# Kernel optimization log

Hardware: AMD Instinct MI355X
Metric: run time of the kernel (lower is better)

Reference implementation:

```python
import jax, jax.numpy as jnp
import numpy as np
import math

B, I, H = 8192, 1024, 1024

def _uniform(key, shape, lo, hi):
    return jax.random.uniform(key, shape, dtype=jnp.float32, minval=lo, maxval=hi)

def setup_inputs() -> dict:
    key = jax.random.key(0)
    ks = jax.random.split(key, 14)
    bound = math.sqrt(1.0 / H)
    lo, hi = -bound, bound
    x = jax.random.normal(ks[0], (B, I), dtype=jnp.float32)
    hid = jax.random.normal(ks[1], (B, H), dtype=jnp.float32)
    # stacked params for gates [r, z, n]
    wx = jnp.stack([_uniform(ks[2 + i], (I, H), lo, hi) for i in range(3)])   # [3, I, H]
    wh = jnp.stack([_uniform(ks[5 + i], (H, H), lo, hi) for i in range(3)])   # [3, H, H]
    bx = jnp.stack([_uniform(ks[8 + i], (H,), lo, hi) for i in range(3)])     # [3, H]
    bh = jnp.stack([_uniform(ks[11 + i], (H,), lo, hi) for i in range(3)])    # [3, H]
    return {"x": x, "hid": hid, "wx": wx, "wh": wh, "bx": bx, "bh": bh}

def reference(x, hid, wx, wh, bx, bh):
    # Fused gate projections: one big matmul per source instead of 3 small ones.
    gx = jnp.einsum('bi,gih->bgh', x, wx) + bx[None]        # [B, 3, H]
    gh = jnp.einsum('bh,ghk->bgk', hid, wh) + bh[None]      # [B, 3, H]
    r = jax.nn.sigmoid(gx[:, 0] + gh[:, 0])
    z = jax.nn.sigmoid(gx[:, 1] + gh[:, 1])
    n = jnp.tanh(gx[:, 2] + r * gh[:, 2])
    next_hid = (1.0 - z) * n + z * hid
    return next_hid
```

## Files before the change

kernel.cpp:

```cpp
#include <hip/hip_runtime.h>
#include <hip/hip_bf16.h>

typedef __hip_bfloat16 bf16;
typedef unsigned short u16;
typedef __attribute__((ext_vector_type(8))) short bf16x8;
typedef __attribute__((ext_vector_type(4))) float f32x4;
typedef __attribute__((ext_vector_type(8))) unsigned short u16x8;

#define KD 1024
#define HD 1024
#define BSZ 8192
#define BM 128
#define BN 64
#define BK 32

#define WS_XB 12582912
#define WS_HB 29360128
#define WS_NEED 46137344ULL

#define NTRB 1536

__device__ __forceinline__ u16 f2b(float f) {
    return __builtin_bit_cast(u16, __float2bfloat16(f));
}

__device__ __forceinline__ void gload16(const void* g, u16* smem, int lds_byte_off) {
    __builtin_amdgcn_global_load_lds(
        (const __attribute__((address_space(1))) void*)g,
        (__attribute__((address_space(3))) void*)((char*)smem + lds_byte_off),
        16, 0, 0);
}

__global__ __launch_bounds__(256) void prep(
    const float* __restrict__ wx, const float* __restrict__ wh, u16* __restrict__ wt,
    const float* __restrict__ x, const float* __restrict__ h,
    u16* __restrict__ xb, u16* __restrict__ hb)
{
    __shared__ float tile[64 * 69];
    const int b = blockIdx.x;
    const int t = threadIdx.x;

    if (b < NTRB) {
        const int g  = b >> 8;
        const int rm = b & 255;
        const int r0 = (rm >> 4) * 64;
        const int c0 = (rm & 15) * 64;
        const float* src = (g < 3) ? (wx + (size_t)g * KD * HD)
                                   : (wh + (size_t)(g - 3) * KD * HD);
        u16* dst = wt + (size_t)g * KD * HD;

        #pragma unroll
        for (int ps = 0; ps < 4; ps++) {
            int idx = ps * 256 + t;
            int row = idx >> 4;
            int c4  = (idx & 15) * 4;
            float4 v = *(const float4*)(src + (size_t)(r0 + row) * HD + c0 + c4);
            *(float4*)&tile[row * 69 + c4] = v;
        }
        __syncthreads();
        const int n = t >> 2;
        #pragma unroll
        for (int p = 0; p < 2; p++) {
            int k0 = (t & 3) * 8 + p * 32;
            u16x8 v;
            #pragma unroll
            for (int e = 0; e < 8; e++)
                v[e] = f2b(tile[(k0 + e) * 69 + n]);
            *(u16x8*)(dst + (size_t)(c0 + n) * KD + r0 + k0) = v;
        }
    } else {
        size_t off = ((size_t)(b - NTRB) * 256 + t) * 8;
        float4 a0 = *(const float4*)(x + off);
        float4 a1 = *(const float4*)(x + off + 4);
        float4 b0 = *(const float4*)(h + off);
        float4 b1 = *(const float4*)(h + off + 4);
        u16x8 vx, vh;
        vx[0]=f2b(a0.x); vx[1]=f2b(a0.y); vx[2]=f2b(a0.z); vx[3]=f2b(a0.w);
        vx[4]=f2b(a1.x); vx[5]=f2b(a1.y); vx[6]=f2b(a1.z); vx[7]=f2b(a1.w);
        vh[0]=f2b(b0.x); vh[1]=f2b(b0.y); vh[2]=f2b(b0.z); vh[3]=f2b(b0.w);
        vh[4]=f2b(b1.x); vh[5]=f2b(b1.y); vh[6]=f2b(b1.z); vh[7]=f2b(b1.w);
        *(u16x8*)(xb + off) = vx;
        *(u16x8*)(hb + off) = vh;
    }
}

__device__ __forceinline__ void gru_epilogue(
    f32x4 (&acc)[4][4][2], const float* __restrict__ bxf, const float* __restrict__ bhf,
    const float* __restrict__ hidf, float* __restrict__ outf,
    int m0, int n0, int wm, int wn, int quad, int c16)
{
    float bR[2], bZ[2], bXN[2], bHN[2];
    #pragma unroll
    for (int j = 0; j < 2; j++) {
        int col = n0 + wn * 32 + j * 16 + c16;
        bR[j]  = bxf[col]          + bhf[col];
        bZ[j]  = bxf[HD + col]     + bhf[HD + col];
        bXN[j] = bxf[2 * HD + col];
        bHN[j] = bhf[2 * HD + col];
    }
    #pragma unroll
    for (int i = 0; i < 4; i++)
        #pragma unroll
        for (int j = 0; j < 2; j++) {
            int col = n0 + wn * 32 + j * 16 + c16;
            #pragma unroll
            for (int r = 0; r < 4; r++) {
                int row = m0 + wm * 64 + i * 16 + quad * 4 + r;
                size_t idx = (size_t)row * HD + col;
                float vr = acc[0][i][j][r] + bR[j];
                vr = 1.f / (1.f + __expf(-vr));
                float vz = acc[1][i][j][r] + bZ[j];
                vz = 1.f / (1.f + __expf(-vz));
                float vn = (acc[2][i][j][r] + bXN[j]) + vr * (acc[3][i][j][r] + bHN[j]);
                float e2 = __expf(2.f * vn);
                vn = 1.f - 2.f / (e2 + 1.f);
                float o = (1.f - vz) * vn + vz * hidf[idx];
                outf[idx] = o;
            }
        }
}

__device__ __forceinline__ void kstep_stage(
    const u16* gx0, const u16* gx1, const u16* gh0, const u16* gh1,
    const u16* gw0, u16* smem, int bufb, int ldsl)
{
    gload16(gx0, smem, bufb + ldsl);
    gload16(gx1, smem, bufb + 4096 + ldsl);
    gload16(gh0, smem, bufb + 8192 + ldsl);
    gload16(gh1, smem, bufb + 12288 + ldsl);
    #pragma unroll
    for (int g = 0; g < 6; g++)
        gload16(gw0 + (size_t)g * KD * HD, smem, bufb + 16384 + g * 4096 + ldsl);
}

__device__ __forceinline__ void kstep_compute(
    const u16* sm, f32x4 (&acc)[4][4][2], int wm, int wn, int quad, int c16)
{
    bf16x8 ax[4], ah[4];
    #pragma unroll
    for (int i = 0; i < 4; i++) {
        int ml = wm * 64 + i * 16 + c16;
        int sl = (quad ^ ((ml >> 1) & 3)) * 8;
        ax[i] = *(const bf16x8*)&sm[ml * BK + sl];
        ah[i] = *(const bf16x8*)&sm[4096 + ml * BK + sl];
    }
    #pragma unroll
    for (int p = 0; p < 3; p++) {
        bf16x8 bwx[2], bwh[2];
        #pragma unroll
        for (int j = 0; j < 2; j++) {
            int nl = wn * 32 + j * 16 + c16;
            int sl = (quad ^ ((nl >> 1) & 3)) * 8;
            bwx[j] = *(const bf16x8*)&sm[8192 + p * 2048       + nl * BK + sl];
            bwh[j] = *(const bf16x8*)&sm[8192 + (p + 3) * 2048 + nl * BK + sl];
        }
        #pragma unroll
        for (int i = 0; i < 4; i++)
            #pragma unroll
            for (int j = 0; j < 2; j++) {
                if (p < 2) {
                    acc[p][i][j] = __builtin_amdgcn_mfma_f32_16x16x32_bf16(ax[i], bwx[j], acc[p][i][j], 0, 0, 0);
                    acc[p][i][j] = __builtin_amdgcn_mfma_f32_16x16x32_bf16(ah[i], bwh[j], acc[p][i][j], 0, 0, 0);
                } else {
                    acc[2][i][j] = __builtin_amdgcn_mfma_f32_16x16x32_bf16(ax[i], bwx[j], acc[2][i][j], 0, 0, 0);
                    acc[3][i][j] = __builtin_amdgcn_mfma_f32_16x16x32_bf16(ah[i], bwh[j], acc[3][i][j], 0, 0, 0);
                }
            }
    }
}

__global__ __launch_bounds__(256, 2) void gru_fused_fast(
    const u16* __restrict__ xb, const u16* __restrict__ hb,
    const u16* __restrict__ wt,
    const float* __restrict__ bxf, const float* __restrict__ bhf,
    const float* __restrict__ hidf, float* __restrict__ outf)
{
    __shared__ u16 smem[40960];
    const int t    = threadIdx.x;
    const int lane = t & 63;
    const int w    = t >> 6;
    const int wm   = w >> 1, wn = w & 1;
    const int quad = lane >> 4;
    const int c16  = lane & 15;
    const int lin  = blockIdx.x;
    const int nblk = (lin & 7) * 2 + ((lin >> 3) & 1);
    const int mblk = lin >> 4;
    const int m0   = mblk * BM;
    const int n0   = nblk * BN;

    const int row4 = t >> 2;
    const int e8s  = ((t & 3) ^ ((t >> 3) & 3)) * 8;
    const u16* gx0 = xb + (size_t)(m0 + row4) * KD + e8s;
    const u16* gx1 = gx0 + (size_t)64 * KD;
    const u16* gh0 = hb + (size_t)(m0 + row4) * KD + e8s;
    const u16* gh1 = gh0 + (size_t)64 * KD;
    const u16* gw0 = wt + (size_t)(n0 + row4) * KD + e8s;
    const int ldsl = w * 1024;

    f32x4 acc[4][4][2];
    #pragma unroll
    for (int a = 0; a < 4; a++)
        #pragma unroll
        for (int i = 0; i < 4; i++)
            #pragma unroll
            for (int j = 0; j < 2; j++)
                acc[a][i][j] = (f32x4){0.f, 0.f, 0.f, 0.f};

    const int NT = KD / BK;

    kstep_stage(gx0, gx1, gh0, gh1, gw0, smem, 0, ldsl);
    gx0 += BK; gx1 += BK; gh0 += BK; gh1 += BK; gw0 += BK;
    __syncthreads();

    for (int tt = 0; tt < NT - 1; ++tt) {
        kstep_stage(gx0, gx1, gh0, gh1, gw0, smem, ((tt + 1) & 1) * 40960, ldsl);
        gx0 += BK; gx1 += BK; gh0 += BK; gh1 += BK; gw0 += BK;
        kstep_compute(smem + (tt & 1) * 20480, acc, wm, wn, quad, c16);
        __syncthreads();
    }
    kstep_compute(smem + 20480, acc, wm, wn, quad, c16);

    gru_epilogue(acc, bxf, bhf, hidf, outf, m0, n0, wm, wn, quad, c16);
}

__global__ __launch_bounds__(256, 2) void gru_fused_slow(
    const float* __restrict__ xf, const float* __restrict__ hf,
    const u16* __restrict__ wt,
    const float* __restrict__ bxf, const float* __restrict__ bhf,
    float* __restrict__ outf)
{
    __shared__ u16 smem[20480];
    const int t    = threadIdx.x;
    const int lane = t & 63;
    const int w    = t >> 6;
    const int wm   = w >> 1, wn = w & 1;
    const int quad = lane >> 4;
    const int c16  = lane & 15;
    const int lin  = blockIdx.x;
    const int nblk = (lin & 7) * 2 + ((lin >> 3) & 1);
    const int mblk = lin >> 4;
    const int m0   = mblk * BM;
    const int n0   = nblk * BN;
    const int row4 = t >> 2;
    const int e8s  = ((t & 3) ^ ((t >> 3) & 3)) * 8;
    const int sls  = e8s;
    const u16* gw0 = wt + (size_t)(n0 + row4) * KD + e8s;
    const int ldsl = w * 1024;

    f32x4 acc[4][4][2];
    #pragma unroll
    for (int a = 0; a < 4; a++)
        #pragma unroll
        for (int i = 0; i < 4; i++)
            #pragma unroll
            for (int j = 0; j < 2; j++)
                acc[a][i][j] = (f32x4){0.f, 0.f, 0.f, 0.f};

    for (int k0 = 0; k0 < KD; k0 += BK) {
        #pragma unroll
        for (int g = 0; g < 6; g++)
            gload16(gw0 + (size_t)g * KD * HD, smem, 16384 + g * 4096 + ldsl);
        gw0 += BK;
        #pragma unroll
        for (int s = 0; s < 2; s++) {
            size_t gidx = (size_t)(m0 + s * 64 + row4) * KD + k0 + (t & 3) * 8;
            const float* px = xf + gidx;
            const float* ph = hf + gidx;
            u16x8 vx, vh;
            #pragma unroll
            for (int e = 0; e < 8; e++) { vx[e] = f2b(px[e]); vh[e] = f2b(ph[e]); }
            *(u16x8*)&smem[s * 2048 + row4 * 32 + sls] = vx;
            *(u16x8*)&smem[4096 + s * 2048 + row4 * 32 + sls] = vh;
        }
        __syncthreads();
        kstep_compute(smem, acc, wm, wn, quad, c16);
        __syncthreads();
    }

    gru_epilogue(acc, bxf, bhf, hf, outf, m0, n0, wm, wn, quad, c16);
}

extern "C" void kernel_launch(void* const* d_in, const int* in_sizes, int n_in,
                              void* d_out, int out_size, void* d_ws, size_t ws_size,
                              hipStream_t stream) {
    const float* x   = (const float*)d_in[0];
    const float* hid = (const float*)d_in[1];
    const float* wx  = (const float*)d_in[2];
    const float* wh  = (const float*)d_in[3];
    const float* bx  = (const float*)d_in[4];
    const float* bh  = (const float*)d_in[5];
    float* out = (float*)d_out;

    char* ws = (char*)d_ws;
    u16* wt = (u16*)ws;
    u16* xb = (u16*)(ws + WS_XB);
    u16* hb = (u16*)(ws + WS_HB);

    if (ws_size >= WS_NEED) {
        prep<<<NTRB + 4096, 256, 0, stream>>>(wx, wh, wt, x, hid, xb, hb);
        gru_fused_fast<<<1024, 256, 0, stream>>>(xb, hb, wt, bx, bh, hid, out);
    } else {
        prep<<<NTRB, 256, 0, stream>>>(wx, wh, wt, x, hid, (u16*)wt, (u16*)wt);
        gru_fused_slow<<<1024, 256, 0, stream>>>(x, hid, wt, bx, bh, out);
    }
}
```

Baseline: 244.8 us.

## Fuse prep and GEMM into one cooperative kernel with grid sync

Replaces the separate prep (weight transpose plus bf16 conversion) and GEMM launches with a single cooperative kernel of 512 blocks. Each block does a share of the transpose and conversion jobs, then all blocks meet at a grid-wide barrier, and each block computes two GEMM tiles. This removes one kernel launch and the gap between kernels. In exchange, the GEMM is limited to a persistent grid of 512 blocks with a grid-sync cost, and it falls back to the two-kernel path if the cooperative launch fails.

```diff
diff --git a/kernel.cpp b/kernel.cpp
--- a/kernel.cpp
+++ b/kernel.cpp
@@ -1,5 +1,8 @@
 #include <hip/hip_runtime.h>
 #include <hip/hip_bf16.h>
+#include <hip/hip_cooperative_groups.h>
+
+namespace cg = cooperative_groups;
 
 typedef __hip_bfloat16 bf16;
 typedef unsigned short u16;
@@ -19,6 +22,7 @@
 #define WS_NEED 46137344ULL
 
 #define NTRB 1536
+#define COOP_GRID 512
 
 __device__ __forceinline__ u16 f2b(float f) {
     return __builtin_bit_cast(u16, __float2bfloat16(f));
@@ -31,57 +35,53 @@
         16, 0, 0);
 }
 
-__global__ __launch_bounds__(256) void prep(
-    const float* __restrict__ wx, const float* __restrict__ wh, u16* __restrict__ wt,
-    const float* __restrict__ x, const float* __restrict__ h,
-    u16* __restrict__ xb, u16* __restrict__ hb)
-{
-    __shared__ float tile[64 * 69];
-    const int b = blockIdx.x;
-    const int t = threadIdx.x;
-
-    if (b < NTRB) {
-        const int g  = b >> 8;
-        const int rm = b & 255;
-        const int r0 = (rm >> 4) * 64;
-        const int c0 = (rm & 15) * 64;
-        const float* src = (g < 3) ? (wx + (size_t)g * KD * HD)
-                                   : (wh + (size_t)(g - 3) * KD * HD);
-        u16* dst = wt + (size_t)g * KD * HD;
-
-        #pragma unroll
-        for (int ps = 0; ps < 4; ps++) {
-            int idx = ps * 256 + t;
-            int row = idx >> 4;
-            int c4  = (idx & 15) * 4;
-            float4 v = *(const float4*)(src + (size_t)(r0 + row) * HD + c0 + c4);
-            *(float4*)&tile[row * 69 + c4] = v;
-        }
-        __syncthreads();
-        const int n = t >> 2;
-        #pragma unroll
-        for (int p = 0; p < 2; p++) {
-            int k0 = (t & 3) * 8 + p * 32;
-            u16x8 v;
-            #pragma unroll
-            for (int e = 0; e < 8; e++)
-                v[e] = f2b(tile[(k0 + e) * 69 + n]);
-            *(u16x8*)(dst + (size_t)(c0 + n) * KD + r0 + k0) = v;
-        }
-    } else {
-        size_t off = ((size_t)(b - NTRB) * 256 + t) * 8;
-        float4 a0 = *(const float4*)(x + off);
-        float4 a1 = *(const float4*)(x + off + 4);
-        float4 b0 = *(const float4*)(h + off);
-        float4 b1 = *(const float4*)(h + off + 4);
-        u16x8 vx, vh;
-        vx[0]=f2b(a0.x); vx[1]=f2b(a0.y); vx[2]=f2b(a0.z); vx[3]=f2b(a0.w);
-        vx[4]=f2b(a1.x); vx[5]=f2b(a1.y); vx[6]=f2b(a1.z); vx[7]=f2b(a1.w);
-        vh[0]=f2b(b0.x); vh[1]=f2b(b0.y); vh[2]=f2b(b0.z); vh[3]=f2b(b0.w);
-        vh[4]=f2b(b1.x); vh[5]=f2b(b1.y); vh[6]=f2b(b1.z); vh[7]=f2b(b1.w);
-        *(u16x8*)(xb + off) = vx;
-        *(u16x8*)(hb + off) = vh;
-    }
+__device__ __forceinline__ void transpose_job(
+    int jj, const float* wx, const float* wh, u16* wt, float* tile, int t)
+{
+    const int g  = jj >> 8;
+    const int rm = jj & 255;
+    const int r0 = (rm >> 4) * 64;
+    const int c0 = (rm & 15) * 64;
+    const float* src = (g < 3) ? (wx + (size_t)g * KD * HD)
+                               : (wh + (size_t)(g - 3) * KD * HD);
+    u16* dst = wt + (size_t)g * KD * HD;
+
+    #pragma unroll
+    for (int ps = 0; ps < 4; ps++) {
+        int idx = ps * 256 + t;
+        int row = idx >> 4;
+        int c4  = (idx & 15) * 4;
+        float4 v = *(const float4*)(src + (size_t)(r0 + row) * HD + c0 + c4);
+        *(float4*)&tile[row * 69 + c4] = v;
+    }
+    __syncthreads();
+    const int n = t >> 2;
+    #pragma unroll
+    for (int p = 0; p < 2; p++) {
+        int k0 = (t & 3) * 8 + p * 32;
+        u16x8 v;
+        #pragma unroll
+        for (int e = 0; e < 8; e++)
+            v[e] = f2b(tile[(k0 + e) * 69 + n]);
+        *(u16x8*)(dst + (size_t)(c0 + n) * KD + r0 + k0) = v;
+    }
+}
+
+__device__ __forceinline__ void convert_job(
+    int cidx, const float* x, const float* h, u16* xb, u16* hb, int t)
+{
+    size_t off = ((size_t)cidx * 256 + t) * 8;
+    float4 a0 = *(const float4*)(x + off);
+    float4 a1 = *(const float4*)(x + off + 4);
+    float4 b0 = *(const float4*)(h + off);
+    float4 b1 = *(const float4*)(h + off + 4);
+    u16x8 vx, vh;
+    vx[0]=f2b(a0.x); vx[1]=f2b(a0.y); vx[2]=f2b(a0.z); vx[3]=f2b(a0.w);
+    vx[4]=f2b(a1.x); vx[5]=f2b(a1.y); vx[6]=f2b(a1.z); vx[7]=f2b(a1.w);
+    vh[0]=f2b(b0.x); vh[1]=f2b(b0.y); vh[2]=f2b(b0.z); vh[3]=f2b(b0.w);
+    vh[4]=f2b(b1.x); vh[5]=f2b(b1.y); vh[6]=f2b(b1.z); vh[7]=f2b(b1.w);
+    *(u16x8*)(xb + off) = vx;
+    *(u16x8*)(hb + off) = vh;
 }
 
 __device__ __forceinline__ void gru_epilogue(
@@ -169,20 +169,16 @@
     }
 }
 
-__global__ __launch_bounds__(256, 2) void gru_fused_fast(
-    const u16* __restrict__ xb, const u16* __restrict__ hb,
-    const u16* __restrict__ wt,
-    const float* __restrict__ bxf, const float* __restrict__ bhf,
-    const float* __restrict__ hidf, float* __restrict__ outf)
-{
-    __shared__ u16 smem[40960];
-    const int t    = threadIdx.x;
+__device__ __forceinline__ void gemm_tile(
+    int lin, u16* smem,
+    const u16* xb, const u16* hb, const u16* wt,
+    const float* bxf, const float* bhf, const float* hidf, float* outf, int t)
+{
     const int lane = t & 63;
     const int w    = t >> 6;
     const int wm   = w >> 1, wn = w & 1;
     const int quad = lane >> 4;
     const int c16  = lane & 15;
-    const int lin  = blockIdx.x;
     const int nblk = (lin & 7) * 2 + ((lin >> 3) & 1);
     const int mblk = lin >> 4;
     const int m0   = mblk * BM;
@@ -221,6 +217,57 @@
     kstep_compute(smem + 20480, acc, wm, wn, quad, c16);
 
     gru_epilogue(acc, bxf, bhf, hidf, outf, m0, n0, wm, wn, quad, c16);
+}
+
+__global__ __launch_bounds__(256, 2) void gru_coop(
+    const float* __restrict__ wx, const float* __restrict__ wh, u16* __restrict__ wt,
+    const float* __restrict__ x, const float* __restrict__ hidf,
+    u16* __restrict__ xb, u16* __restrict__ hb,
+    const float* __restrict__ bxf, const float* __restrict__ bhf,
+    float* __restrict__ outf)
+{
+    __shared__ u16 smem[40960];
+    const int t = threadIdx.x;
+    const int b = blockIdx.x;
+
+    {
+        float* tile = (float*)smem;
+        #pragma unroll
+        for (int i = 0; i < 3; i++) {
+            if (i) __syncthreads();
+            transpose_job(b + COOP_GRID * i, wx, wh, wt, tile, t);
+        }
+        #pragma unroll
+        for (int i = 0; i < 8; i++)
+            convert_job(b + COOP_GRID * i, x, hidf, xb, hb, t);
+    }
+    __threadfence();
+    cg::this_grid().sync();
+
+    gemm_tile(b,             smem, xb, hb, wt, bxf, bhf, hidf, outf, t);
+    gemm_tile(b + COOP_GRID, smem, xb, hb, wt, bxf, bhf, hidf, outf, t);
+}
+
+__global__ __launch_bounds__(256) void prep(
+    const float* __restrict__ wx, const float* __restrict__ wh, u16* __restrict__ wt,
+    const float* __restrict__ x, const float* __restrict__ h,
+    u16* __restrict__ xb, u16* __restrict__ hb)
+{
+    __shared__ float tile[64 * 69];
+    const int b = blockIdx.x;
+    const int t = threadIdx.x;
+    if (b < NTRB) transpose_job(b, wx, wh, wt, tile, t);
+    else          convert_job(b - NTRB, x, h, xb, hb, t);
+}
+
+__global__ __launch_bounds__(256, 2) void gru_fused_fast(
+    const u16* __restrict__ xb, const u16* __restrict__ hb,
+    const u16* __restrict__ wt,
+    const float* __restrict__ bxf, const float* __restrict__ bhf,
+    const float* __restrict__ hidf, float* __restrict__ outf)
+{
+    __shared__ u16 smem[40960];
+    gemm_tile(blockIdx.x, smem, xb, hb, wt, bxf, bhf, hidf, outf, threadIdx.x);
 }
 
 __global__ __launch_bounds__(256, 2) void gru_fused_slow(
@@ -243,7 +290,6 @@
     const int n0   = nblk * BN;
     const int row4 = t >> 2;
     const int e8s  = ((t & 3) ^ ((t >> 3) & 3)) * 8;
-    const int sls  = e8s;
     const u16* gw0 = wt + (size_t)(n0 + row4) * KD + e8s;
     const int ldsl = w * 1024;
 
@@ -269,8 +315,8 @@
             u16x8 vx, vh;
             #pragma unroll
             for (int e = 0; e < 8; e++) { vx[e] = f2b(px[e]); vh[e] = f2b(ph[e]); }
-            *(u16x8*)&smem[s * 2048 + row4 * 32 + sls] = vx;
-            *(u16x8*)&smem[4096 + s * 2048 + row4 * 32 + sls] = vh;
+            *(u16x8*)&smem[s * 2048 + row4 * 32 + e8s] = vx;
+            *(u16x8*)&smem[4096 + s * 2048 + row4 * 32 + e8s] = vh;
         }
         __syncthreads();
         kstep_compute(smem, acc, wm, wn, quad, c16);
@@ -297,8 +343,17 @@
     u16* hb = (u16*)(ws + WS_HB);
 
     if (ws_size >= WS_NEED) {
-        prep<<<NTRB + 4096, 256, 0, stream>>>(wx, wh, wt, x, hid, xb, hb);
-        gru_fused_fast<<<1024, 256, 0, stream>>>(xb, hb, wt, bx, bh, hid, out);
+        void* args[] = {
+            (void*)&wx, (void*)&wh, (void*)&wt, (void*)&x, (void*)&hid,
+            (void*)&xb, (void*)&hb, (void*)&bx, (void*)&bh, (void*)&out
+        };
+        hipError_t err = hipLaunchCooperativeKernel(
+            (const void*)gru_coop, dim3(COOP_GRID), dim3(256), args, 0, stream);
+        if (err != hipSuccess) {
+            (void)hipGetLastError();
+            prep<<<NTRB + 4096, 256, 0, stream>>>(wx, wh, wt, x, hid, xb, hb);
+            gru_fused_fast<<<1024, 256, 0, stream>>>(xb, hb, wt, bx, bh, hid, out);
+        }
     } else {
         prep<<<NTRB, 256, 0, stream>>>(wx, wh, wt, x, hid, (u16*)wt, (u16*)wt);
         gru_fused_slow<<<1024, 256, 0, stream>>>(x, hid, wt, bx, bh, out);
```

New measurement: 386.6 us. 57.9% more time.

## Load weight fragments directly from global into registers, stage only activations in LDS

Applied to the files above, without the earlier changes.

The fast kernel stops staging the six weight tiles through shared memory. Each lane now loads its B-operand fragments for all gates straight from global memory into registers every k-step, while only the x/h activations stay double-buffered in LDS, which shrinks LDS from 80KB to 32KB. The goal is to cut LDS traffic and footprint. In exchange, each k-step issues uncoalesced-ish global loads with little latency hiding before the MFMAs, and weights are re-read by every wave that shares them.

```diff
diff --git a/kernel.cpp b/kernel.cpp
--- a/kernel.cpp
+++ b/kernel.cpp
@@ -13,6 +13,7 @@
 #define BM 128
 #define BN 64
 #define BK 32
+#define NT (KD / BK)
 
 #define WS_XB 12582912
 #define WS_HB 29360128
@@ -120,50 +121,22 @@
         }
 }
 
-__device__ __forceinline__ void kstep_stage(
-    const u16* gx0, const u16* gx1, const u16* gh0, const u16* gh1,
-    const u16* gw0, u16* smem, int bufb, int ldsl)
-{
-    gload16(gx0, smem, bufb + ldsl);
-    gload16(gx1, smem, bufb + 4096 + ldsl);
-    gload16(gh0, smem, bufb + 8192 + ldsl);
-    gload16(gh1, smem, bufb + 12288 + ldsl);
-    #pragma unroll
-    for (int g = 0; g < 6; g++)
-        gload16(gw0 + (size_t)g * KD * HD, smem, bufb + 16384 + g * 4096 + ldsl);
-}
-
-__device__ __forceinline__ void kstep_compute(
-    const u16* sm, f32x4 (&acc)[4][4][2], int wm, int wn, int quad, int c16)
-{
-    bf16x8 ax[4], ah[4];
-    #pragma unroll
-    for (int i = 0; i < 4; i++) {
-        int ml = wm * 64 + i * 16 + c16;
-        int sl = (quad ^ ((ml >> 1) & 3)) * 8;
-        ax[i] = *(const bf16x8*)&sm[ml * BK + sl];
-        ah[i] = *(const bf16x8*)&sm[4096 + ml * BK + sl];
-    }
+__device__ __forceinline__ void mfma_all(
+    const bf16x8 (&ax)[4], const bf16x8 (&ah)[4], const bf16x8 (&bw)[6][2],
+    f32x4 (&acc)[4][4][2])
+{
     #pragma unroll
     for (int p = 0; p < 3; p++) {
-        bf16x8 bwx[2], bwh[2];
-        #pragma unroll
-        for (int j = 0; j < 2; j++) {
-            int nl = wn * 32 + j * 16 + c16;
-            int sl = (quad ^ ((nl >> 1) & 3)) * 8;
-            bwx[j] = *(const bf16x8*)&sm[8192 + p * 2048       + nl * BK + sl];
-            bwh[j] = *(const bf16x8*)&sm[8192 + (p + 3) * 2048 + nl * BK + sl];
-        }
         #pragma unroll
         for (int i = 0; i < 4; i++)
             #pragma unroll
             for (int j = 0; j < 2; j++) {
                 if (p < 2) {
-                    acc[p][i][j] = __builtin_amdgcn_mfma_f32_16x16x32_bf16(ax[i], bwx[j], acc[p][i][j], 0, 0, 0);
-                    acc[p][i][j] = __builtin_amdgcn_mfma_f32_16x16x32_bf16(ah[i], bwh[j], acc[p][i][j], 0, 0, 0);
+                    acc[p][i][j] = __builtin_amdgcn_mfma_f32_16x16x32_bf16(ax[i], bw[p][j],     acc[p][i][j], 0, 0, 0);
+                    acc[p][i][j] = __builtin_amdgcn_mfma_f32_16x16x32_bf16(ah[i], bw[p + 3][j], acc[p][i][j], 0, 0, 0);
                 } else {
-                    acc[2][i][j] = __builtin_amdgcn_mfma_f32_16x16x32_bf16(ax[i], bwx[j], acc[2][i][j], 0, 0, 0);
-                    acc[3][i][j] = __builtin_amdgcn_mfma_f32_16x16x32_bf16(ah[i], bwh[j], acc[3][i][j], 0, 0, 0);
+                    acc[2][i][j] = __builtin_amdgcn_mfma_f32_16x16x32_bf16(ax[i], bw[2][j], acc[2][i][j], 0, 0, 0);
+                    acc[3][i][j] = __builtin_amdgcn_mfma_f32_16x16x32_bf16(ah[i], bw[5][j], acc[3][i][j], 0, 0, 0);
                 }
             }
     }
@@ -175,7 +148,7 @@
     const float* __restrict__ bxf, const float* __restrict__ bhf,
     const float* __restrict__ hidf, float* __restrict__ outf)
 {
-    __shared__ u16 smem[40960];
+    __shared__ u16 smem[16384];
     const int t    = threadIdx.x;
     const int lane = t & 63;
     const int w    = t >> 6;
@@ -194,8 +167,10 @@
     const u16* gx1 = gx0 + (size_t)64 * KD;
     const u16* gh0 = hb + (size_t)(m0 + row4) * KD + e8s;
     const u16* gh1 = gh0 + (size_t)64 * KD;
-    const u16* gw0 = wt + (size_t)(n0 + row4) * KD + e8s;
     const int ldsl = w * 1024;
+
+    const u16* pb0 = wt + (size_t)(n0 + wn * 32 + c16) * KD + quad * 8;
+    const u16* pb1 = pb0 + (size_t)16 * KD;
 
     f32x4 acc[4][4][2];
     #pragma unroll
@@ -206,21 +181,83 @@
             for (int j = 0; j < 2; j++)
                 acc[a][i][j] = (f32x4){0.f, 0.f, 0.f, 0.f};
 
-    const int NT = KD / BK;
-
-    kstep_stage(gx0, gx1, gh0, gh1, gw0, smem, 0, ldsl);
-    gx0 += BK; gx1 += BK; gh0 += BK; gh1 += BK; gw0 += BK;
+    gload16(gx0, smem, 0     + ldsl);
+    gload16(gx1, smem, 4096  + ldsl);
+    gload16(gh0, smem, 8192  + ldsl);
+    gload16(gh1, smem, 12288 + ldsl);
+    gx0 += BK; gx1 += BK; gh0 += BK; gh1 += BK;
     __syncthreads();
 
-    for (int tt = 0; tt < NT - 1; ++tt) {
-        kstep_stage(gx0, gx1, gh0, gh1, gw0, smem, ((tt + 1) & 1) * 40960, ldsl);
-        gx0 += BK; gx1 += BK; gh0 += BK; gh1 += BK; gw0 += BK;
-        kstep_compute(smem + (tt & 1) * 20480, acc, wm, wn, quad, c16);
-        __syncthreads();
-    }
-    kstep_compute(smem + 20480, acc, wm, wn, quad, c16);
+    for (int tt = 0; tt < NT; ++tt) {
+        bf16x8 bw[6][2];
+        #pragma unroll
+        for (int g = 0; g < 6; g++) {
+            bw[g][0] = *(const bf16x8*)(pb0 + (size_t)g * KD * HD);
+            bw[g][1] = *(const bf16x8*)(pb1 + (size_t)g * KD * HD);
+        }
+        pb0 += BK; pb1 += BK;
+
+        if (tt < NT - 1) {
+            int bufb = ((tt + 1) & 1) * 16384;
+            gload16(gx0, smem, bufb + ldsl);
+            gload16(gx1, smem, bufb + 4096 + ldsl);
+            gload16(gh0, smem, bufb + 8192 + ldsl);
+            gload16(gh1, smem, bufb + 12288 + ldsl);
+            gx0 += BK; gx1 += BK; gh0 += BK; gh1 += BK;
+        }
+
+        const u16* sm = smem + (tt & 1) * 8192;
+        bf16x8 ax[4], ah[4];
+        #pragma unroll
+        for (int i = 0; i < 4; i++) {
+            int ml = wm * 64 + i * 16 + c16;
+            int sl = (quad ^ ((ml >> 1) & 3)) * 8;
+            ax[i] = *(const bf16x8*)&sm[ml * BK + sl];
+            ah[i] = *(const bf16x8*)&sm[4096 + ml * BK + sl];
+        }
+
+        mfma_all(ax, ah, bw, acc);
+
+        if (tt < NT - 1) __syncthreads();
+    }
 
     gru_epilogue(acc, bxf, bhf, hidf, outf, m0, n0, wm, wn, quad, c16);
+}
+
+__device__ __forceinline__ void kstep_compute_lds(
+    const u16* sm, f32x4 (&acc)[4][4][2], int wm, int wn, int quad, int c16)
+{
+    bf16x8 ax[4], ah[4];
+    #pragma unroll
+    for (int i = 0; i < 4; i++) {
+        int ml = wm * 64 + i * 16 + c16;
+        int sl = (quad ^ ((ml >> 1) & 3)) * 8;
+        ax[i] = *(const bf16x8*)&sm[ml * BK + sl];
+        ah[i] = *(const bf16x8*)&sm[4096 + ml * BK + sl];
+    }
+    #pragma unroll
+    for (int p = 0; p < 3; p++) {
+        bf16x8 bwx[2], bwh[2];
+        #pragma unroll
+        for (int j = 0; j < 2; j++) {
+            int nl = wn * 32 + j * 16 + c16;
+            int sl = (quad ^ ((nl >> 1) & 3)) * 8;
+            bwx[j] = *(const bf16x8*)&sm[8192 + p * 2048       + nl * BK + sl];
+            bwh[j] = *(const bf16x8*)&sm[8192 + (p + 3) * 2048 + nl * BK + sl];
+        }
+        #pragma unroll
+        for (int i = 0; i < 4; i++)
+            #pragma unroll
+            for (int j = 0; j < 2; j++) {
+                if (p < 2) {
+                    acc[p][i][j] = __builtin_amdgcn_mfma_f32_16x16x32_bf16(ax[i], bwx[j], acc[p][i][j], 0, 0, 0);
+                    acc[p][i][j] = __builtin_amdgcn_mfma_f32_16x16x32_bf16(ah[i], bwh[j], acc[p][i][j], 0, 0, 0);
+                } else {
+                    acc[2][i][j] = __builtin_amdgcn_mfma_f32_16x16x32_bf16(ax[i], bwx[j], acc[2][i][j], 0, 0, 0);
+                    acc[3][i][j] = __builtin_amdgcn_mfma_f32_16x16x32_bf16(ah[i], bwh[j], acc[3][i][j], 0, 0, 0);
+                }
+            }
+    }
 }
 
 __global__ __launch_bounds__(256, 2) void gru_fused_slow(
@@ -243,7 +280,6 @@
     const int n0   = nblk * BN;
     const int row4 = t >> 2;
     const int e8s  = ((t & 3) ^ ((t >> 3) & 3)) * 8;
-    const int sls  = e8s;
     const u16* gw0 = wt + (size_t)(n0 + row4) * KD + e8s;
     const int ldsl = w * 1024;
 
@@ -269,11 +305,11 @@
             u16x8 vx, vh;
             #pragma unroll
             for (int e = 0; e < 8; e++) { vx[e] = f2b(px[e]); vh[e] = f2b(ph[e]); }
-            *(u16x8*)&smem[s * 2048 + row4 * 32 + sls] = vx;
-            *(u16x8*)&smem[4096 + s * 2048 + row4 * 32 + sls] = vh;
+            *(u16x8*)&smem[s * 2048 + row4 * 32 + e8s] = vx;
+            *(u16x8*)&smem[4096 + s * 2048 + row4 * 32 + e8s] = vh;
         }
         __syncthreads();
-        kstep_compute(smem, acc, wm, wn, quad, c16);
+        kstep_compute_lds(smem, acc, wm, wn, quad, c16);
         __syncthreads();
     }
 
```

Result: slower. 330.4 us (+34.9%).
